# Optimization experiments

Hardware: AMD Instinct MI355X
Metric: run time of the kernel (lower is better)

The kernel has to match this reference:

```python
import jax, jax.numpy as jnp
import numpy as np

TEMP = 1.0

def setup_inputs() -> dict:
    key = jax.random.key(0)
    k1, k2, k3, k4 = jax.random.split(key, 4)
    B, Q, K, H = 8, 1024, 4096, 512
    output = jax.random.normal(k1, (B, Q, H), dtype=jnp.float32)
    context = jax.random.normal(k2, (B, K, H), dtype=jnp.float32)
    mask = jax.random.randint(k3, (B, Q, K), 0, 2).astype(jnp.bool_)
    # linear_out: Linear(2H -> H), torch layout W: [H, 2H]
    W_out = jax.random.normal(k4, (H, 2 * H), dtype=jnp.float32) * (1.0 / np.sqrt(2 * H))
    b_out = jnp.zeros((H,), dtype=jnp.float32)
    return {"output": output, "context": context, "mask": mask, "W_out": W_out, "b_out": b_out}

def reference(output, context, mask, W_out, b_out):
    # attn scores: [B, Q, K]
    attn = jnp.einsum('bqh,bkh->bqk', output, context)
    attn = jnp.where(mask, -jnp.inf, attn)
    attn = jax.nn.softmax(attn / TEMP, axis=-1)
    # mix: [B, Q, H]
    mix = jnp.einsum('bqk,bkh->bqh', attn, context)
    combined = jnp.concatenate([mix, output], axis=-1)  # [B, Q, 2H]
    out = jnp.tanh(jnp.einsum('bqc,hc->bqh', combined, W_out) + b_out)
    return (out, attn)
```

## Files before the change

kernel.cpp:

```cpp
#include <hip/hip_runtime.h>
#include <cstdint>
#include <cstddef>

#define B_N 8
#define Q_N 1024
#define K_N 4096
#define H_N 512
#define C_N 1024
#define R_N (B_N * Q_N)

typedef short bf16x8 __attribute__((ext_vector_type(8)));
typedef float f32x4 __attribute__((ext_vector_type(4)));

typedef const void __attribute__((address_space(1))) gas_void;
typedef void __attribute__((address_space(3))) las_void;

__device__ __forceinline__ unsigned short f2bf(float f) {
    union { float f; unsigned u; } v; v.f = f;
    unsigned u = v.u;
    u += 0x7FFFu + ((u >> 16) & 1u);
    return (unsigned short)(u >> 16);
}
__device__ __forceinline__ float bf2f(unsigned short h) {
    union { unsigned u; float f; } v; v.u = ((unsigned)h) << 16;
    return v.f;
}

__device__ __forceinline__ f32x4 mfma16(bf16x8 a, bf16x8 b, f32x4 c) {
    return __builtin_amdgcn_mfma_f32_16x16x32_bf16(a, b, c, 0, 0, 0);
}

__global__ void k_split(const float* __restrict__ x, unsigned short* __restrict__ hi,
                        unsigned short* __restrict__ lo, int n4) {
    int i = blockIdx.x * 256 + threadIdx.x;
    if (i >= n4) return;
    float4 v = reinterpret_cast<const float4*>(x)[i];
    ushort4 h, l;
    h.x = f2bf(v.x); l.x = f2bf(v.x - bf2f(h.x));
    h.y = f2bf(v.y); l.y = f2bf(v.y - bf2f(h.y));
    h.z = f2bf(v.z); l.z = f2bf(v.z - bf2f(h.z));
    h.w = f2bf(v.w); l.w = f2bf(v.w - bf2f(h.w));
    reinterpret_cast<ushort4*>(hi)[i] = h;
    reinterpret_cast<ushort4*>(lo)[i] = l;
}

__global__ void k_cvt(const float* __restrict__ x, unsigned short* __restrict__ hi, int n4) {
    int i = blockIdx.x * 256 + threadIdx.x;
    if (i >= n4) return;
    float4 v = reinterpret_cast<const float4*>(x)[i];
    ushort4 h;
    h.x = f2bf(v.x); h.y = f2bf(v.y); h.z = f2bf(v.z); h.w = f2bf(v.w);
    reinterpret_cast<ushort4*>(hi)[i] = h;
}

__global__ __launch_bounds__(256)
void k_prep_ctx(const float* __restrict__ ctx, unsigned short* __restrict__ ctxHi,
                unsigned short* __restrict__ ctxLo, unsigned short* __restrict__ ctxT) {
    __shared__ unsigned short tile[64][66];
    const int b = blockIdx.z;
    const int k0 = blockIdx.x * 64;
    const int h0 = blockIdx.y * 64;
    const int tx = threadIdx.x & 15;
    const int ty = threadIdx.x >> 4;
#pragma unroll
    for (int r = 0; r < 64; r += 16) {
        const int k = ty + r;
        const size_t go = ((size_t)b * K_N + k0 + k) * H_N + h0 + tx * 4;
        float4 v = *reinterpret_cast<const float4*>(ctx + go);
        ushort4 h, l;
        h.x = f2bf(v.x); l.x = f2bf(v.x - bf2f(h.x));
        h.y = f2bf(v.y); l.y = f2bf(v.y - bf2f(h.y));
        h.z = f2bf(v.z); l.z = f2bf(v.z - bf2f(h.z));
        h.w = f2bf(v.w); l.w = f2bf(v.w - bf2f(h.w));
        *reinterpret_cast<ushort4*>(ctxHi + go) = h;
        *reinterpret_cast<ushort4*>(ctxLo + go) = l;
        tile[tx * 4 + 0][k] = h.x;
        tile[tx * 4 + 1][k] = h.y;
        tile[tx * 4 + 2][k] = h.z;
        tile[tx * 4 + 3][k] = h.w;
    }
    __syncthreads();
#pragma unroll
    for (int r = 0; r < 64; r += 16) {
        const int h = ty + r;
        ushort4 t4 = *reinterpret_cast<const ushort4*>(&tile[h][tx * 4]);
        *reinterpret_cast<ushort4*>(ctxT + ((size_t)b * H_N + h0 + h) * K_N + k0 + tx * 4) = t4;
    }
}

__device__ __forceinline__ void stage_tile(const unsigned short* __restrict__ g, int ld,
                                           unsigned short* __restrict__ lds) {
    const int t = threadIdx.x;
    const int wbase = t & ~63;
#pragma unroll
    for (int i = 0; i < 2; i++) {
        int idx = i * 256 + t;
        const unsigned short* ga = g + (size_t)(idx >> 2) * ld + (idx & 3) * 8;
        unsigned short* la = lds + (size_t)(i * 256 + wbase) * 8;
        __builtin_amdgcn_global_load_lds((gas_void*)ga, (las_void*)la, 16, 0, 0);
    }
}
__device__ __forceinline__ void stage_tile64(const unsigned short* __restrict__ g, int ld,
                                             unsigned short* __restrict__ lds) {
    const int t = threadIdx.x;
    const unsigned short* ga = g + (size_t)(t >> 2) * ld + (t & 3) * 8;
    unsigned short* la = lds + (size_t)(t & ~63) * 8;
    __builtin_amdgcn_global_load_lds((gas_void*)ga, (las_void*)la, 16, 0, 0);
}

__global__ __launch_bounds__(256, 2)
void k_scores(const unsigned short* __restrict__ outHi, const unsigned short* __restrict__ outLo,
              const unsigned short* __restrict__ ctxHi, const unsigned short* __restrict__ ctxLo,
              float* __restrict__ S) {
    __shared__ unsigned short Ah[128 * 32], Al[128 * 32], Bh[128 * 32], Bl[128 * 32];
    const int b = blockIdx.z;
    const int q0 = blockIdx.y * 128;
    const int k0 = blockIdx.x * 128;
    const unsigned short* Ahg = outHi + ((size_t)b * Q_N + q0) * H_N;
    const unsigned short* Alg = outLo + ((size_t)b * Q_N + q0) * H_N;
    const unsigned short* Bhg = ctxHi + ((size_t)b * K_N + k0) * H_N;
    const unsigned short* Blg = ctxLo + ((size_t)b * K_N + k0) * H_N;
    const int lane = threadIdx.x & 63;
    const int w = threadIdx.x >> 6;
    const int wr = (w >> 1) * 64;
    const int wc = (w & 1) * 64;
    const int fm = lane & 15;
    const int fg = (lane >> 4) * 8;

    f32x4 acc[4][4];
#pragma unroll
    for (int i = 0; i < 4; i++)
#pragma unroll
        for (int j = 0; j < 4; j++) acc[i][j] = (f32x4){0.f, 0.f, 0.f, 0.f};

    for (int kc = 0; kc < H_N; kc += 32) {
        stage_tile(Ahg + kc, H_N, Ah);
        stage_tile(Alg + kc, H_N, Al);
        stage_tile(Bhg + kc, H_N, Bh);
        stage_tile(Blg + kc, H_N, Bl);
        __syncthreads();
        bf16x8 ah[4], al[4], bh[4], bl[4];
#pragma unroll
        for (int i = 0; i < 4; i++) {
            ah[i] = *(const bf16x8*)&Ah[(wr + i * 16 + fm) * 32 + fg];
            al[i] = *(const bf16x8*)&Al[(wr + i * 16 + fm) * 32 + fg];
            bh[i] = *(const bf16x8*)&Bh[(wc + i * 16 + fm) * 32 + fg];
            bl[i] = *(const bf16x8*)&Bl[(wc + i * 16 + fm) * 32 + fg];
        }
#pragma unroll
        for (int i = 0; i < 4; i++)
#pragma unroll
            for (int j = 0; j < 4; j++) {
                acc[i][j] = mfma16(ah[i], bh[j], acc[i][j]);
                acc[i][j] = mfma16(ah[i], bl[j], acc[i][j]);
                acc[i][j] = mfma16(al[i], bh[j], acc[i][j]);
            }
        __syncthreads();
    }
    float* Sb = S + (size_t)b * Q_N * K_N;
    const int orow = (lane >> 4) * 4;
    const int ocol = lane & 15;
#pragma unroll
    for (int i = 0; i < 4; i++)
#pragma unroll
        for (int r = 0; r < 4; r++) {
            int q = q0 + wr + i * 16 + orow + r;
            float* dst = Sb + (size_t)q * K_N + (k0 + wc + ocol);
#pragma unroll
            for (int j = 0; j < 4; j++) dst[j * 16] = acc[i][j][r];
        }
}

__global__ __launch_bounds__(256)
void k_softmax(float* __restrict__ S, const int* __restrict__ mask, unsigned short* __restrict__ pbf) {
    const size_t r = blockIdx.x;
    float* row = S + r * K_N;
    const int* mrow = mask + r * K_N;
    unsigned short* prow = pbf + r * K_N;
    const int t = threadIdx.x;

    float4 v[4];
    float lmax = -1e30f;
#pragma unroll
    for (int i = 0; i < 4; i++) {
        int idx = i * 256 + t;
        float4 s = reinterpret_cast<const float4*>(row)[idx];
        int4 mk = reinterpret_cast<const int4*>(mrow)[idx];
        s.x = mk.x ? -1e30f : s.x;
        s.y = mk.y ? -1e30f : s.y;
        s.z = mk.z ? -1e30f : s.z;
        s.w = mk.w ? -1e30f : s.w;
        v[i] = s;
        lmax = fmaxf(fmaxf(fmaxf(lmax, s.x), fmaxf(s.y, s.z)), s.w);
    }
#pragma unroll
    for (int off = 32; off >= 1; off >>= 1)
        lmax = fmaxf(lmax, __shfl_xor(lmax, off, 64));
    __shared__ float redm[4];
    __shared__ float reds[4];
    const int wv = t >> 6;
    if ((t & 63) == 0) redm[wv] = lmax;
    __syncthreads();
    const float m = fmaxf(fmaxf(redm[0], redm[1]), fmaxf(redm[2], redm[3]));

    float4 e[4];
    float lsum = 0.f;
#pragma unroll
    for (int i = 0; i < 4; i++) {
        e[i].x = __expf(v[i].x - m);
        e[i].y = __expf(v[i].y - m);
        e[i].z = __expf(v[i].z - m);
        e[i].w = __expf(v[i].w - m);
        lsum += (e[i].x + e[i].y) + (e[i].z + e[i].w);
    }
#pragma unroll
    for (int off = 32; off >= 1; off >>= 1)
        lsum += __shfl_xor(lsum, off, 64);
    if ((t & 63) == 0) reds[wv] = lsum;
    __syncthreads();
    const float inv = 1.0f / (reds[0] + reds[1] + reds[2] + reds[3]);

#pragma unroll
    for (int i = 0; i < 4; i++) {
        int idx = i * 256 + t;
        float4 p;
        p.x = e[i].x * inv; p.y = e[i].y * inv; p.z = e[i].z * inv; p.w = e[i].w * inv;
        reinterpret_cast<float4*>(row)[idx] = p;
        ushort4 pb;
        pb.x = f2bf(p.x); pb.y = f2bf(p.y); pb.z = f2bf(p.z); pb.w = f2bf(p.w);
        reinterpret_cast<ushort4*>(prow)[idx] = pb;
    }
}

__global__ __launch_bounds__(256, 2)
void k_mix(const unsigned short* __restrict__ P, const unsigned short* __restrict__ ctxT,
           unsigned short* __restrict__ mixBf) {
    __shared__ unsigned short A0[128 * 32], A1[128 * 32], B0[64 * 32], B1[64 * 32];
    const int b = blockIdx.z;
    const int q0 = blockIdx.y * 128;
    const int h0 = blockIdx.x * 64;
    const unsigned short* Ag = P + ((size_t)b * Q_N + q0) * K_N;
    const unsigned short* Bg = ctxT + ((size_t)b * H_N + h0) * K_N;
    const int lane = threadIdx.x & 63;
    const int w = threadIdx.x >> 6;
    const int wr = w * 32;
    const int fm = lane & 15;
    const int fg = (lane >> 4) * 8;

    f32x4 acc[2][4];
#pragma unroll
    for (int i = 0; i < 2; i++)
#pragma unroll
        for (int j = 0; j < 4; j++) acc[i][j] = (f32x4){0.f, 0.f, 0.f, 0.f};

    for (int kc = 0; kc < K_N; kc += 64) {
        stage_tile(Ag + kc, K_N, A0);
        stage_tile(Ag + kc + 32, K_N, A1);
        stage_tile64(Bg + kc, K_N, B0);
        stage_tile64(Bg + kc + 32, K_N, B1);
        __syncthreads();
        bf16x8 a[2], bb[4];
#pragma unroll
        for (int i = 0; i < 2; i++) a[i] = *(const bf16x8*)&A0[(wr + i * 16 + fm) * 32 + fg];
#pragma unroll
        for (int j = 0; j < 4; j++) bb[j] = *(const bf16x8*)&B0[(j * 16 + fm) * 32 + fg];
#pragma unroll
        for (int i = 0; i < 2; i++)
#pragma unroll
            for (int j = 0; j < 4; j++) acc[i][j] = mfma16(a[i], bb[j], acc[i][j]);
#pragma unroll
        for (int i = 0; i < 2; i++) a[i] = *(const bf16x8*)&A1[(wr + i * 16 + fm) * 32 + fg];
#pragma unroll
        for (int j = 0; j < 4; j++) bb[j] = *(const bf16x8*)&B1[(j * 16 + fm) * 32 + fg];
#pragma unroll
        for (int i = 0; i < 2; i++)
#pragma unroll
            for (int j = 0; j < 4; j++) acc[i][j] = mfma16(a[i], bb[j], acc[i][j]);
        __syncthreads();
    }
    const int orow = (lane >> 4) * 4;
    const int ocol = lane & 15;
#pragma unroll
    for (int i = 0; i < 2; i++)
#pragma unroll
        for (int r = 0; r < 4; r++) {
            int q = q0 + wr + i * 16 + orow + r;
            unsigned short* dst = mixBf + ((size_t)b * Q_N + q) * H_N + (h0 + ocol);
#pragma unroll
            for (int j = 0; j < 4; j++) dst[j * 16] = f2bf(acc[i][j][r]);
        }
}

__global__ __launch_bounds__(256, 2)
void k_outlin(const unsigned short* __restrict__ mixBf, const unsigned short* __restrict__ outHi,
              const unsigned short* __restrict__ Whi, const float* __restrict__ bias,
              float* __restrict__ out) {
    __shared__ unsigned short At[128 * 32], Bt[64 * 32];
    const int r0 = blockIdx.y * 128;
    const int h0 = blockIdx.x * 64;
    const int lane = threadIdx.x & 63;
    const int w = threadIdx.x >> 6;
    const int wr = w * 32;
    const int fm = lane & 15;
    const int fg = (lane >> 4) * 8;

    f32x4 acc[2][4];
#pragma unroll
    for (int i = 0; i < 2; i++)
#pragma unroll
        for (int j = 0; j < 4; j++) acc[i][j] = (f32x4){0.f, 0.f, 0.f, 0.f};

    for (int kc = 0; kc < C_N; kc += 32) {
        const unsigned short* Ag = (kc < H_N)
            ? mixBf + (size_t)r0 * H_N + kc
            : outHi + (size_t)r0 * H_N + (kc - H_N);
        stage_tile(Ag, H_N, At);
        stage_tile64(Whi + (size_t)h0 * C_N + kc, C_N, Bt);
        __syncthreads();
        bf16x8 a[2], bb[4];
#pragma unroll
        for (int i = 0; i < 2; i++) a[i] = *(const bf16x8*)&At[(wr + i * 16 + fm) * 32 + fg];
#pragma unroll
        for (int j = 0; j < 4; j++) bb[j] = *(const bf16x8*)&Bt[(j * 16 + fm) * 32 + fg];
#pragma unroll
        for (int i = 0; i < 2; i++)
#pragma unroll
            for (int j = 0; j < 4; j++) acc[i][j] = mfma16(a[i], bb[j], acc[i][j]);
        __syncthreads();
    }
    const int orow = (lane >> 4) * 4;
    const int ocol = lane & 15;
#pragma unroll
    for (int i = 0; i < 2; i++)
#pragma unroll
        for (int r = 0; r < 4; r++) {
            int rr = r0 + wr + i * 16 + orow + r;
#pragma unroll
            for (int j = 0; j < 4; j++) {
                int h = h0 + j * 16 + ocol;
                float v = acc[i][j][r] + bias[h];
                out[(size_t)rr * H_N + h] = tanhf(v);
            }
        }
}

extern "C" void kernel_launch(void* const* d_in, const int* in_sizes, int n_in,
                              void* d_out, int out_size, void* d_ws, size_t ws_size,
                              hipStream_t stream) {
    const float* d_output  = (const float*)d_in[0];
    const float* d_context = (const float*)d_in[1];
    const int*   d_mask    = (const int*)d_in[2];
    const float* d_W       = (const float*)d_in[3];
    const float* d_bias    = (const float*)d_in[4];

    float* out_res = (float*)d_out;
    float* attn    = out_res + (size_t)R_N * H_N;

    char* ws = (char*)d_ws;
    unsigned short* ctxHi = (unsigned short*)ws; ws += (size_t)B_N * K_N * H_N * 2;
    unsigned short* ctxLo = (unsigned short*)ws; ws += (size_t)B_N * K_N * H_N * 2;
    unsigned short* ctxT  = (unsigned short*)ws; ws += (size_t)B_N * K_N * H_N * 2;
    unsigned short* outHi = (unsigned short*)ws; ws += (size_t)R_N * H_N * 2;
    unsigned short* outLo = (unsigned short*)ws; ws += (size_t)R_N * H_N * 2;
    unsigned short* Whi   = (unsigned short*)ws; ws += (size_t)H_N * C_N * 2;
    unsigned short* pBf   = (unsigned short*)ws; ws += (size_t)R_N * K_N * 2;
    unsigned short* mixBf = (unsigned short*)ws; ws += (size_t)R_N * H_N * 2;

    k_split<<<dim3((R_N * H_N / 4) / 256), 256, 0, stream>>>(d_output, outHi, outLo, R_N * H_N / 4);
    k_cvt<<<dim3((H_N * C_N / 4) / 256), 256, 0, stream>>>(d_W, Whi, H_N * C_N / 4);
    k_prep_ctx<<<dim3(K_N / 64, H_N / 64, B_N), 256, 0, stream>>>(d_context, ctxHi, ctxLo, ctxT);

    k_scores<<<dim3(K_N / 128, Q_N / 128, B_N), 256, 0, stream>>>(outHi, outLo, ctxHi, ctxLo, attn);

    k_softmax<<<dim3(R_N), 256, 0, stream>>>(attn, d_mask, pBf);

    k_mix<<<dim3(H_N / 64, Q_N / 128, B_N), 256, 0, stream>>>(pBf, ctxT, mixBf);

    k_outlin<<<dim3(H_N / 64, R_N / 128), 256, 0, stream>>>(mixBf, outHi, Whi, d_bias, out_res);
}
```

Baseline: 557.2 us.

## Enlarge mix GEMM tile to 128x128 with split-K and fused prep conversions

```diff
diff --git a/kernel.cpp b/kernel.cpp
--- a/kernel.cpp
+++ b/kernel.cpp
@@ -30,27 +30,30 @@
     return __builtin_amdgcn_mfma_f32_16x16x32_bf16(a, b, c, 0, 0, 0);
 }
 
-__global__ void k_split(const float* __restrict__ x, unsigned short* __restrict__ hi,
-                        unsigned short* __restrict__ lo, int n4) {
+__global__ void k_split_cvt(const float* __restrict__ outp, unsigned short* __restrict__ outHi,
+                            unsigned short* __restrict__ outLo, const float* __restrict__ W,
+                            unsigned short* __restrict__ Whi) {
+    const int n4a = R_N * H_N / 4;
+    const int n4b = H_N * C_N / 4;
     int i = blockIdx.x * 256 + threadIdx.x;
-    if (i >= n4) return;
-    float4 v = reinterpret_cast<const float4*>(x)[i];
-    ushort4 h, l;
-    h.x = f2bf(v.x); l.x = f2bf(v.x - bf2f(h.x));
-    h.y = f2bf(v.y); l.y = f2bf(v.y - bf2f(h.y));
-    h.z = f2bf(v.z); l.z = f2bf(v.z - bf2f(h.z));
-    h.w = f2bf(v.w); l.w = f2bf(v.w - bf2f(h.w));
-    reinterpret_cast<ushort4*>(hi)[i] = h;
-    reinterpret_cast<ushort4*>(lo)[i] = l;
-}
-
-__global__ void k_cvt(const float* __restrict__ x, unsigned short* __restrict__ hi, int n4) {
-    int i = blockIdx.x * 256 + threadIdx.x;
-    if (i >= n4) return;
-    float4 v = reinterpret_cast<const float4*>(x)[i];
-    ushort4 h;
-    h.x = f2bf(v.x); h.y = f2bf(v.y); h.z = f2bf(v.z); h.w = f2bf(v.w);
-    reinterpret_cast<ushort4*>(hi)[i] = h;
+    if (i < n4a) {
+        float4 v = reinterpret_cast<const float4*>(outp)[i];
+        ushort4 h, l;
+        h.x = f2bf(v.x); l.x = f2bf(v.x - bf2f(h.x));
+        h.y = f2bf(v.y); l.y = f2bf(v.y - bf2f(h.y));
+        h.z = f2bf(v.z); l.z = f2bf(v.z - bf2f(h.z));
+        h.w = f2bf(v.w); l.w = f2bf(v.w - bf2f(h.w));
+        reinterpret_cast<ushort4*>(outHi)[i] = h;
+        reinterpret_cast<ushort4*>(outLo)[i] = l;
+    } else {
+        int j = i - n4a;
+        if (j < n4b) {
+            float4 v = reinterpret_cast<const float4*>(W)[j];
+            ushort4 h;
+            h.x = f2bf(v.x); h.y = f2bf(v.y); h.z = f2bf(v.z); h.w = f2bf(v.w);
+            reinterpret_cast<ushort4*>(Whi)[j] = h;
+        }
+    }
 }
 
 __global__ __launch_bounds__(256)
@@ -234,61 +237,79 @@
 
 __global__ __launch_bounds__(256, 2)
 void k_mix(const unsigned short* __restrict__ P, const unsigned short* __restrict__ ctxT,
-           unsigned short* __restrict__ mixBf) {
-    __shared__ unsigned short A0[128 * 32], A1[128 * 32], B0[64 * 32], B1[64 * 32];
-    const int b = blockIdx.z;
+           float* __restrict__ part) {
+    __shared__ unsigned short A0[128 * 32], A1[128 * 32], B0[128 * 32], B1[128 * 32];
+    const int b = blockIdx.z >> 1;
+    const int s = blockIdx.z & 1;
+    const int kBase = s * (K_N / 2);
     const int q0 = blockIdx.y * 128;
-    const int h0 = blockIdx.x * 64;
+    const int h0 = blockIdx.x * 128;
     const unsigned short* Ag = P + ((size_t)b * Q_N + q0) * K_N;
     const unsigned short* Bg = ctxT + ((size_t)b * H_N + h0) * K_N;
     const int lane = threadIdx.x & 63;
     const int w = threadIdx.x >> 6;
-    const int wr = w * 32;
+    const int wr = (w >> 1) * 64;
+    const int wc = (w & 1) * 64;
     const int fm = lane & 15;
     const int fg = (lane >> 4) * 8;
 
-    f32x4 acc[2][4];
-#pragma unroll
-    for (int i = 0; i < 2; i++)
+    f32x4 acc[4][4];
+#pragma unroll
+    for (int i = 0; i < 4; i++)
 #pragma unroll
         for (int j = 0; j < 4; j++) acc[i][j] = (f32x4){0.f, 0.f, 0.f, 0.f};
 
-    for (int kc = 0; kc < K_N; kc += 64) {
+    for (int kc = kBase; kc < kBase + K_N / 2; kc += 64) {
         stage_tile(Ag + kc, K_N, A0);
         stage_tile(Ag + kc + 32, K_N, A1);
-        stage_tile64(Bg + kc, K_N, B0);
-        stage_tile64(Bg + kc + 32, K_N, B1);
-        __syncthreads();
-        bf16x8 a[2], bb[4];
-#pragma unroll
-        for (int i = 0; i < 2; i++) a[i] = *(const bf16x8*)&A0[(wr + i * 16 + fm) * 32 + fg];
-#pragma unroll
-        for (int j = 0; j < 4; j++) bb[j] = *(const bf16x8*)&B0[(j * 16 + fm) * 32 + fg];
-#pragma unroll
-        for (int i = 0; i < 2; i++)
+        stage_tile(Bg + kc, K_N, B0);
+        stage_tile(Bg + kc + 32, K_N, B1);
+        __syncthreads();
+        bf16x8 a[4], bb[4];
+#pragma unroll
+        for (int i = 0; i < 4; i++) {
+            a[i] = *(const bf16x8*)&A0[(wr + i * 16 + fm) * 32 + fg];
+            bb[i] = *(const bf16x8*)&B0[(wc + i * 16 + fm) * 32 + fg];
+        }
+#pragma unroll
+        for (int i = 0; i < 4; i++)
 #pragma unroll
             for (int j = 0; j < 4; j++) acc[i][j] = mfma16(a[i], bb[j], acc[i][j]);
 #pragma unroll
-        for (int i = 0; i < 2; i++) a[i] = *(const bf16x8*)&A1[(wr + i * 16 + fm) * 32 + fg];
-#pragma unroll
-        for (int j = 0; j < 4; j++) bb[j] = *(const bf16x8*)&B1[(j * 16 + fm) * 32 + fg];
-#pragma unroll
-        for (int i = 0; i < 2; i++)
+        for (int i = 0; i < 4; i++) {
+            a[i] = *(const bf16x8*)&A1[(wr + i * 16 + fm) * 32 + fg];
+            bb[i] = *(const bf16x8*)&B1[(wc + i * 16 + fm) * 32 + fg];
+        }
+#pragma unroll
+        for (int i = 0; i < 4; i++)
 #pragma unroll
             for (int j = 0; j < 4; j++) acc[i][j] = mfma16(a[i], bb[j], acc[i][j]);
         __syncthreads();
     }
+    float* dst0 = part + (size_t)s * R_N * H_N;
     const int orow = (lane >> 4) * 4;
     const int ocol = lane & 15;
 #pragma unroll
-    for (int i = 0; i < 2; i++)
+    for (int i = 0; i < 4; i++)
 #pragma unroll
         for (int r = 0; r < 4; r++) {
             int q = q0 + wr + i * 16 + orow + r;
-            unsigned short* dst = mixBf + ((size_t)b * Q_N + q) * H_N + (h0 + ocol);
-#pragma unroll
-            for (int j = 0; j < 4; j++) dst[j * 16] = f2bf(acc[i][j][r]);
-        }
+            float* dst = dst0 + ((size_t)b * Q_N + q) * H_N + (h0 + wc + ocol);
+#pragma unroll
+            for (int j = 0; j < 4; j++) dst[j * 16] = acc[i][j][r];
+        }
+}
+
+__global__ void k_reduce(const float* __restrict__ part, unsigned short* __restrict__ mixBf) {
+    int i = blockIdx.x * 256 + threadIdx.x;
+    const float4 a = reinterpret_cast<const float4*>(part)[i];
+    const float4 b = reinterpret_cast<const float4*>(part + (size_t)R_N * H_N)[i];
+    ushort4 h;
+    h.x = f2bf(a.x + b.x);
+    h.y = f2bf(a.y + b.y);
+    h.z = f2bf(a.z + b.z);
+    h.w = f2bf(a.w + b.w);
+    reinterpret_cast<ushort4*>(mixBf)[i] = h;
 }
 
 __global__ __launch_bounds__(256, 2)
@@ -366,15 +387,18 @@
     unsigned short* pBf   = (unsigned short*)ws; ws += (size_t)R_N * K_N * 2;
     unsigned short* mixBf = (unsigned short*)ws; ws += (size_t)R_N * H_N * 2;
 
-    k_split<<<dim3((R_N * H_N / 4) / 256), 256, 0, stream>>>(d_output, outHi, outLo, R_N * H_N / 4);
-    k_cvt<<<dim3((H_N * C_N / 4) / 256), 256, 0, stream>>>(d_W, Whi, H_N * C_N / 4);
+    float* part = (float*)ctxHi;
+
+    const int n4_sc = R_N * H_N / 4 + H_N * C_N / 4;
+    k_split_cvt<<<dim3((n4_sc + 255) / 256), 256, 0, stream>>>(d_output, outHi, outLo, d_W, Whi);
     k_prep_ctx<<<dim3(K_N / 64, H_N / 64, B_N), 256, 0, stream>>>(d_context, ctxHi, ctxLo, ctxT);
 
     k_scores<<<dim3(K_N / 128, Q_N / 128, B_N), 256, 0, stream>>>(outHi, outLo, ctxHi, ctxLo, attn);
 
     k_softmax<<<dim3(R_N), 256, 0, stream>>>(attn, d_mask, pBf);
 
-    k_mix<<<dim3(H_N / 64, Q_N / 128, B_N), 256, 0, stream>>>(pBf, ctxT, mixBf);
+    k_mix<<<dim3(H_N / 128, Q_N / 128, B_N * 2), 256, 0, stream>>>(pBf, ctxT, part);
+    k_reduce<<<dim3((R_N * H_N / 4) / 256), 256, 0, stream>>>(part, mixBf);
 
     k_outlin<<<dim3(H_N / 64, R_N / 128), 256, 0, stream>>>(mixBf, outHi, Whi, d_bias, out_res);
 }
```

Result: faster. 539.4 us (-3.2%).
